# Kernel tuning notes

Measured on AMD Instinct MI355X. Metric: run time of the kernel, lower is better.

## Reference

```python
import jax, jax.numpy as jnp
import numpy as np

HID = 512       # hidden_dim (embed/LSTM input)
HDE = 512       # hidden_dim_de == attn_channels (required by conv_att channel count)
NCLS = 7000
LSEQ = 40
B = 128
FH, FW = 8, 32


def setup_inputs() -> dict:
    key = jax.random.key(0)
    ks = jax.random.split(key, 16)
    s = 0.05
    inp = {
        "hidden_en": jax.random.normal(ks[0], (1, B, HID), jnp.float32),
        "x_em": jax.random.normal(ks[1], (B, HDE, FH, FW), jnp.float32),
        "att_x_em": jax.random.normal(ks[2], (B, FH * FW, HDE), jnp.float32),
        "target": jax.random.randint(ks[3], (B, LSEQ), 0, NCLS),
        "feature_h": FH,
        "feature_w": FW,
        # parameters
        "embed_w": jax.random.normal(ks[4], (NCLS, HID), jnp.float32) * s,
        "W_ih": jax.random.normal(ks[5], (4 * HDE, HID), jnp.float32) * s,   # LSTMCell input weights (i,f,g,o)
        "W_hh": jax.random.normal(ks[6], (4 * HDE, HDE), jnp.float32) * s,
        "b_ih": jax.random.normal(ks[7], (4 * HDE,), jnp.float32) * s,
        "b_hh": jax.random.normal(ks[8], (4 * HDE,), jnp.float32) * s,
        "hem_w": jax.random.normal(ks[9], (HDE, HDE), jnp.float32) * s,     # 1x1 conv h_em as matrix
        "hem_b": jax.random.normal(ks[10], (HDE,), jnp.float32) * s,
        "attw_w": jax.random.normal(ks[11], (HDE,), jnp.float32) * s,       # 1x1 conv conv_att -> 1 channel
        "attw_b": jax.random.normal(ks[12], (), jnp.float32) * s,
        "lin_w": jax.random.normal(ks[13], (NCLS, HDE + HDE), jnp.float32) * s,
        "lin_b": jax.random.normal(ks[14], (NCLS,), jnp.float32) * s,
    }
    return inp


def _decode(hidden_en, x_em, att_x_em, target, embed_w, W_ih, W_hh, b_ih, b_hh,
            hem_w, hem_b, attw_w, attw_b, lin_w, lin_b):
    L = target.shape[1]
    # teacher-forced inputs: step 0 uses hidden_en[-1], step t>=1 uses embed(target[:, t-1])
    xt0 = hidden_en[-1]                                   # [B, HID]
    xts = jnp.concatenate([xt0[None], jnp.transpose(embed_w[target[:, : L - 1]], (1, 0, 2))], axis=0)  # [L,B,HID]
    xg_all = jnp.einsum('lbi,gi->lbg', xts, W_ih) + b_ih  # precompute input gates [L,B,4H]
    Bn = x_em.shape[0]
    h0 = jnp.zeros((Bn, HDE), x_em.dtype)
    c0 = jnp.zeros((Bn, HDE), x_em.dtype)

    def step(carry, xg):
        h, c = carry
        gates = xg + h @ W_hh.T + b_hh
        i, f, g, o = jnp.split(gates, 4, axis=-1)
        c = jax.nn.sigmoid(f) * c + jax.nn.sigmoid(i) * jnp.tanh(g)
        h = jax.nn.sigmoid(o) * jnp.tanh(c)
        # additive attention (dropout treated as identity for determinism)
        hem = h @ hem_w.T + hem_b                          # [B, C]
        feat = jnp.tanh(x_em + hem[:, :, None, None])      # [B, C, H, W]
        feat_att = jnp.einsum('bchw,c->bhw', feat, attw_w) + attw_b
        alpha = jax.nn.softmax(feat_att.reshape(Bn, -1), axis=-1)  # [B, HW]
        att = jnp.einsum('bn,bnd->bd', alpha, att_x_em)    # [B, C]
        scores = jax.nn.log_softmax(jnp.concatenate([h, att], -1) @ lin_w.T + lin_b)
        return (h, c), scores

    _, ys = jax.lax.scan(step, (h0, c0), xg_all)           # ys: [L, B, NCLS]
    return jnp.transpose(ys, (1, 0, 2))                    # [B, L, NCLS]


def reference(hidden_en, x_em, att_x_em, target, feature_h, feature_w,
              embed_w, W_ih, W_hh, b_ih, b_hh, hem_w, hem_b, attw_w, attw_b,
              lin_w, lin_b):
    return _decode(hidden_en, x_em, att_x_em, target, embed_w, W_ih, W_hh,
                   b_ih, b_hh, hem_w, hem_b, attw_w, attw_b, lin_w, lin_b)
```

## Files before the change

### kernel.cpp

```cpp
#include <hip/hip_runtime.h>

#define B_    128
#define HIDD  512
#define NCLS  7000
#define NPAD  7040
#define LSEQ  40
#define MROWS 5120
#define TT    10

typedef __attribute__((ext_vector_type(8))) short bf16x8;
typedef __attribute__((ext_vector_type(4))) float f32x4;

__device__ __forceinline__ unsigned short f2bf(float x) {
  union { float f; unsigned u; } v; v.f = x;
  unsigned r = v.u + 0x7fffu + ((v.u >> 16) & 1u);
  return (unsigned short)(r >> 16);
}
__device__ __forceinline__ float bf2f(unsigned short h) {
  union { unsigned u; float f; } v; v.u = ((unsigned)h) << 16;
  return v.f;
}
__device__ __forceinline__ float sigm(float x) { return 1.f / (1.f + __expf(-x)); }
__device__ __forceinline__ float tanh_f(float x) {
  float e = __expf(2.f * x);
  return 1.f - 2.f / (e + 1.f);
}
__device__ __forceinline__ float rcp_f(float x) { return __builtin_amdgcn_rcpf(x); }

__global__ __launch_bounds__(256) void k_cvt(const float* __restrict__ src,
                                             unsigned short* __restrict__ dst, int n4) {
  int i = blockIdx.x * 256 + threadIdx.x;
  if (i >= n4) return;
  float4 v = ((const float4*)src)[i];
  ushort4 o; o.x = f2bf(v.x); o.y = f2bf(v.y); o.z = f2bf(v.z); o.w = f2bf(v.w);
  ((ushort4*)dst)[i] = o;
}

__global__ __launch_bounds__(256) void k_expcvt(const float* __restrict__ src,
                                                unsigned short* __restrict__ dst, int n4) {
  int i = blockIdx.x * 256 + threadIdx.x;
  if (i >= n4) return;
  float4 v = ((const float4*)src)[i];
  ushort4 o;
  o.x = f2bf(__expf(2.f * v.x)); o.y = f2bf(__expf(2.f * v.y));
  o.z = f2bf(__expf(2.f * v.z)); o.w = f2bf(__expf(2.f * v.w));
  ((ushort4*)dst)[i] = o;
}

__global__ __launch_bounds__(256) void k_linpad(const float* __restrict__ lw,
                                                unsigned short* __restrict__ dst) {
  int i = blockIdx.x * 256 + threadIdx.x;
  int e = i * 4;
  int row = e >> 10;
  ushort4 o;
  if (row < NCLS) {
    float4 v = *(const float4*)(lw + (size_t)row * 1024 + (e & 1023));
    o.x = f2bf(v.x); o.y = f2bf(v.y); o.z = f2bf(v.z); o.w = f2bf(v.w);
  } else { o.x = 0; o.y = 0; o.z = 0; o.w = 0; }
  ((ushort4*)dst)[i] = o;
}

__global__ __launch_bounds__(256) void k_xts(const float* __restrict__ hidden_en,
                                             const float* __restrict__ embed_w,
                                             const int* __restrict__ target,
                                             unsigned short* __restrict__ xts) {
  int i = blockIdx.x * 256 + threadIdx.x;
  int e = i * 4;
  int r = e >> 9, col = e & 511;
  int l = r >> 7, b = r & 127;
  const float* src;
  if (l == 0) src = hidden_en + b * 512 + col;
  else        src = embed_w + (size_t)target[b * LSEQ + (l - 1)] * 512 + col;
  float4 v = *(const float4*)src;
  ushort4 o; o.x = f2bf(v.x); o.y = f2bf(v.y); o.z = f2bf(v.z); o.w = f2bf(v.w);
  ((ushort4*)xts)[i] = o;
}

template <int MODE>
__global__ __launch_bounds__(256) void k_gemm(const unsigned short* __restrict__ A, int lda,
                                              const unsigned short* __restrict__ Bw, int ldb,
                                              const float* __restrict__ bias,
                                              void* __restrict__ outp, int ldc, int K) {
  __shared__ __align__(16) unsigned short As[128 * 32];
  __shared__ __align__(16) unsigned short Bs[128 * 32];
  const int tid = threadIdx.x;
  const int lane = tid & 63, wid = tid >> 6;
  const int wm = wid >> 1, wn = wid & 1;
  const int quad = lane >> 4, l16 = lane & 15;
  const int m0 = blockIdx.x * 128, n0 = blockIdx.y * 128;
  f32x4 acc[4][4];
#pragma unroll
  for (int i = 0; i < 4; i++)
#pragma unroll
    for (int j = 0; j < 4; j++) acc[i][j] = (f32x4){0.f, 0.f, 0.f, 0.f};

  const int r0 = tid >> 2, kq0 = (tid & 3) * 8;
  for (int k0 = 0; k0 < K; k0 += 32) {
#pragma unroll
    for (int s = 0; s < 2; s++) {
      int row = r0 + s * 64;
      *(bf16x8*)(As + row * 32 + kq0) = *(const bf16x8*)(A + (size_t)(m0 + row) * lda + k0 + kq0);
      *(bf16x8*)(Bs + row * 32 + kq0) = *(const bf16x8*)(Bw + (size_t)(n0 + row) * ldb + k0 + kq0);
    }
    __syncthreads();
    bf16x8 af[4], bfr[4];
#pragma unroll
    for (int i = 0; i < 4; i++)
      af[i] = *(const bf16x8*)(As + (wm * 64 + i * 16 + l16) * 32 + quad * 8);
#pragma unroll
    for (int j = 0; j < 4; j++)
      bfr[j] = *(const bf16x8*)(Bs + (wn * 64 + j * 16 + l16) * 32 + quad * 8);
#pragma unroll
    for (int i = 0; i < 4; i++)
#pragma unroll
      for (int j = 0; j < 4; j++)
        acc[i][j] = __builtin_amdgcn_mfma_f32_16x16x32_bf16(af[i], bfr[j], acc[i][j], 0, 0, 0);
    __syncthreads();
  }
#pragma unroll
  for (int i = 0; i < 4; i++) {
    int mbase = m0 + wm * 64 + i * 16 + quad * 4;
#pragma unroll
    for (int j = 0; j < 4; j++) {
      int n = n0 + wn * 64 + j * 16 + l16;
#pragma unroll
      for (int r = 0; r < 4; r++) {
        float v = acc[i][j][r];
        int m = mbase + r;
        if (MODE == 0) {
          ((unsigned short*)outp)[(size_t)m * ldc + n] = f2bf(v + bias[n]);
        } else if (MODE == 3) {
          ((float*)outp)[(size_t)m * ldc + n] = __expf(2.f * (v + bias[n]));
        } else {
          if (n < NCLS) {
            int t = m >> 7, b = m & 127;
            ((float*)outp)[((size_t)(b * LSEQ + t)) * NCLS + n] = v + bias[n];
          }
        }
      }
    }
  }
}

__global__ __launch_bounds__(256) void k_gates(const float* __restrict__ h_prev,
                                               float* __restrict__ h_new,
                                               float* __restrict__ c_buf,
                                               const unsigned short* __restrict__ xg,
                                               const float* __restrict__ W_hh,
                                               const float* __restrict__ b_hh,
                                               unsigned short* __restrict__ hatt, int t) {
  __shared__ float h_s[16][68];
  __shared__ float W_s[64][68];
  const int tid = threadIdx.x;
  const int mt = blockIdx.x >> 5, jt = blockIdx.x & 31;
  const int m0 = mt * 16, j0 = jt * 16;
  const int mi = tid >> 4, ji = tid & 15;
  float a0 = 0.f, a1 = 0.f, a2 = 0.f, a3 = 0.f;
  if (t > 0) {
    for (int k0 = 0; k0 < 512; k0 += 64) {
      {
        int row = tid >> 4, c4 = (tid & 15) * 4;
        *(float4*)&h_s[row][c4] = *(const float4*)&h_prev[(m0 + row) * 512 + k0 + c4];
      }
#pragma unroll
      for (int w = 0; w < 4; w++) {
        int lin = w * 256 + tid;
        int row = lin >> 4, c4 = (lin & 15) * 4;
        int g = row >> 4, jj = row & 15;
        *(float4*)&W_s[row][c4] = *(const float4*)&W_hh[(size_t)((g << 9) + j0 + jj) * 512 + k0 + c4];
      }
      __syncthreads();
#pragma unroll 4
      for (int kk = 0; kk < 64; kk += 4) {
        float4 hv = *(const float4*)&h_s[mi][kk];
        float4 w0 = *(const float4*)&W_s[ji][kk];
        float4 w1 = *(const float4*)&W_s[16 + ji][kk];
        float4 w2 = *(const float4*)&W_s[32 + ji][kk];
        float4 w3 = *(const float4*)&W_s[48 + ji][kk];
        a0 += hv.x * w0.x + hv.y * w0.y + hv.z * w0.z + hv.w * w0.w;
        a1 += hv.x * w1.x + hv.y * w1.y + hv.z * w1.z + hv.w * w1.w;
        a2 += hv.x * w2.x + hv.y * w2.y + hv.z * w2.z + hv.w * w2.w;
        a3 += hv.x * w3.x + hv.y * w3.y + hv.z * w3.z + hv.w * w3.w;
      }
      __syncthreads();
    }
  }
  const int m = m0 + mi, j = j0 + ji;
  const size_t r = (size_t)t * 128 + m;
  a0 += bf2f(xg[r * 2048 + j])          + b_hh[j];
  a1 += bf2f(xg[r * 2048 + 512 + j])    + b_hh[512 + j];
  a2 += bf2f(xg[r * 2048 + 1024 + j])   + b_hh[1024 + j];
  a3 += bf2f(xg[r * 2048 + 1536 + j])   + b_hh[1536 + j];
  float ig = sigm(a0), fg = sigm(a1), gg = tanh_f(a2), og = sigm(a3);
  float c_old = (t > 0) ? c_buf[m * 512 + j] : 0.f;
  float c = fg * c_old + ig * gg;
  float h = og * tanh_f(c);
  c_buf[m * 512 + j] = c;
  h_new[m * 512 + j] = h;
  hatt[r * 1024 + j] = f2bf(h);
}

__global__ __launch_bounds__(256) void k_feat(const float* __restrict__ Eh,
                                              const unsigned short* __restrict__ Ex,
                                              const float* __restrict__ attw_w,
                                              float* __restrict__ s_all) {
  __shared__ float EhL[TT][512];
  __shared__ float wL[512];
  const int tid = threadIdx.x;
  const int tg = blockIdx.x >> 7, b = blockIdx.x & 127;
  const int t0 = tg * TT;
  for (int i = tid * 4; i < TT * 512; i += 1024) {
    int t = i >> 9, c = i & 511;
    *(float4*)&EhL[t][c] = *(const float4*)&Eh[((size_t)(t0 + t) * 128 + b) * 512 + c];
  }
  if (tid < 128) *(float4*)&wL[tid * 4] = *(const float4*)&attw_w[tid * 4];
  __syncthreads();
  const int p = tid;
  const unsigned short* xp = Ex + (size_t)b * 512 * 256 + p;
  float acc[TT];
#pragma unroll
  for (int t = 0; t < TT; t++) acc[t] = 0.f;
  for (int c0 = 0; c0 < 512; c0 += 4) {
    float ex0 = bf2f(xp[(size_t)(c0 + 0) * 256]);
    float ex1 = bf2f(xp[(size_t)(c0 + 1) * 256]);
    float ex2 = bf2f(xp[(size_t)(c0 + 2) * 256]);
    float ex3 = bf2f(xp[(size_t)(c0 + 3) * 256]);
    float4 wv = *(const float4*)&wL[c0];
#pragma unroll
    for (int t = 0; t < TT; t++) {
      float4 eh = *(const float4*)&EhL[t][c0];
      acc[t] = __builtin_fmaf(wv.x, rcp_f(__builtin_fmaf(ex0, eh.x, 1.f)), acc[t]);
      acc[t] = __builtin_fmaf(wv.y, rcp_f(__builtin_fmaf(ex1, eh.y, 1.f)), acc[t]);
      acc[t] = __builtin_fmaf(wv.z, rcp_f(__builtin_fmaf(ex2, eh.z, 1.f)), acc[t]);
      acc[t] = __builtin_fmaf(wv.w, rcp_f(__builtin_fmaf(ex3, eh.w, 1.f)), acc[t]);
    }
  }
#pragma unroll
  for (int t = 0; t < TT; t++)
    s_all[((size_t)(t0 + t) * 128 + b) * 256 + p] = -2.f * acc[t];
}

__global__ __launch_bounds__(256) void k_att(const float* __restrict__ s_all,
                                             const float* __restrict__ atx,
                                             unsigned short* __restrict__ hatt) {
  __shared__ float sL[40][257];
  __shared__ float zinv[40];
  const int tid = threadIdx.x;
  const int b = blockIdx.x >> 1, dh = blockIdx.x & 1;
  for (int i = tid; i < 40 * 256; i += 256) {
    int t = i >> 8, p = i & 255;
    sL[t][p] = s_all[((size_t)t * 128 + b) * 256 + p];
  }
  __syncthreads();
  if (tid < 40) {
    int t = tid;
    float mx = -1e30f;
    for (int p = 0; p < 256; p++) mx = fmaxf(mx, sL[t][p]);
    float z = 0.f;
    for (int p = 0; p < 256; p++) { float e = __expf(sL[t][p] - mx); sL[t][p] = e; z += e; }
    zinv[t] = 1.f / z;
  }
  __syncthreads();
  float acc[40];
#pragma unroll
  for (int t = 0; t < 40; t++) acc[t] = 0.f;
  const int d = dh * 256 + tid;
  const float* ap = atx + (size_t)b * 256 * 512 + d;
  for (int p = 0; p < 256; p++) {
    float av = ap[(size_t)p * 512];
#pragma unroll
    for (int t = 0; t < 40; t++) acc[t] += sL[t][p] * av;
  }
#pragma unroll
  for (int t = 0; t < 40; t++) {
    float v = acc[t] * zinv[t];
    hatt[((size_t)t * 128 + b) * 1024 + 512 + d] = f2bf(v);
  }
}

__global__ __launch_bounds__(256) void k_lsm(float* __restrict__ out) {
  __shared__ float buf[7000];
  __shared__ float red[256];
  const int tid = threadIdx.x;
  float* pr = out + (size_t)blockIdx.x * NCLS;
  for (int i = tid * 4; i < NCLS; i += 1024)
    *(float4*)&buf[i] = *(const float4*)&pr[i];
  __syncthreads();
  float mx = -1e30f;
  for (int i = tid; i < NCLS; i += 256) mx = fmaxf(mx, buf[i]);
  red[tid] = mx; __syncthreads();
  for (int s = 128; s > 0; s >>= 1) { if (tid < s) red[tid] = fmaxf(red[tid], red[tid + s]); __syncthreads(); }
  mx = red[0]; __syncthreads();
  float sum = 0.f;
  for (int i = tid; i < NCLS; i += 256) sum += __expf(buf[i] - mx);
  red[tid] = sum; __syncthreads();
  for (int s = 128; s > 0; s >>= 1) { if (tid < s) red[tid] += red[tid + s]; __syncthreads(); }
  float lse = mx + __logf(red[0]);
  for (int i = tid * 4; i < NCLS; i += 1024) {
    float4 v = *(const float4*)&buf[i];
    v.x -= lse; v.y -= lse; v.z -= lse; v.w -= lse;
    *(float4*)&pr[i] = v;
  }
}

extern "C" void kernel_launch(void* const* d_in, const int* in_sizes, int n_in,
                              void* d_out, int out_size, void* d_ws, size_t ws_size,
                              hipStream_t stream) {
  const float* hidden_en = (const float*)d_in[0];
  const float* x_em      = (const float*)d_in[1];
  const float* att_x     = (const float*)d_in[2];
  const int*   target    = (const int*)d_in[3];
  const float* embed_w   = (const float*)d_in[6];
  const float* W_ih      = (const float*)d_in[7];
  const float* W_hh      = (const float*)d_in[8];
  const float* b_ih      = (const float*)d_in[9];
  const float* b_hh      = (const float*)d_in[10];
  const float* hem_w     = (const float*)d_in[11];
  const float* hem_b     = (const float*)d_in[12];
  const float* attw_w    = (const float*)d_in[13];
  const float* lin_w     = (const float*)d_in[15];
  const float* lin_b     = (const float*)d_in[16];
  float* out = (float*)d_out;
  (void)in_sizes; (void)n_in; (void)out_size; (void)ws_size;

  char* w = (char*)d_ws;
  size_t off = 0;
  auto alloc = [&](size_t bytes) { char* p = w + off; off = (off + bytes + 255) & ~(size_t)255; return p; };
  unsigned short* xts  = (unsigned short*)alloc((size_t)MROWS * 512 * 2);
  unsigned short* wih  = (unsigned short*)alloc((size_t)2048 * 512 * 2);
  unsigned short* xg   = (unsigned short*)alloc((size_t)MROWS * 2048 * 2);
  unsigned short* hemw = (unsigned short*)alloc((size_t)512 * 512 * 2);
  unsigned short* linw = (unsigned short*)alloc((size_t)NPAD * 1024 * 2);
  unsigned short* xem  = (unsigned short*)alloc((size_t)128 * 512 * 256 * 2);
  unsigned short* hatt = (unsigned short*)alloc((size_t)MROWS * 1024 * 2);
  float* h0      = (float*)alloc((size_t)128 * 512 * 4);
  float* h1      = (float*)alloc((size_t)128 * 512 * 4);
  float* cb      = (float*)alloc((size_t)128 * 512 * 4);
  float* eh_all  = (float*)alloc((size_t)MROWS * 512 * 4);
  float* s_all   = (float*)alloc((size_t)MROWS * 256 * 4);

  k_cvt<<<1024, 256, 0, stream>>>(W_ih, wih, 2048 * 512 / 4);
  k_cvt<<<256, 256, 0, stream>>>(hem_w, hemw, 512 * 512 / 4);
  k_expcvt<<<16384, 256, 0, stream>>>(x_em, xem, 128 * 512 * 256 / 4);
  k_linpad<<<NPAD * 1024 / 4 / 256, 256, 0, stream>>>(lin_w, linw);
  k_xts<<<MROWS * 512 / 4 / 256, 256, 0, stream>>>(hidden_en, embed_w, target, xts);
  k_gemm<0><<<dim3(40, 16), 256, 0, stream>>>(xts, 512, wih, 512, b_ih, xg, 2048, 512);

  for (int t = 0; t < LSEQ; t++) {
    const float* hp = (t & 1) ? h0 : h1;
    float* hn = (t & 1) ? h1 : h0;
    k_gates<<<256, 256, 0, stream>>>(hp, hn, cb, xg, W_hh, b_hh, hatt, t);
  }

  k_gemm<3><<<dim3(40, 4), 256, 0, stream>>>(hatt, 1024, hemw, 512, hem_b, eh_all, 512, 512);
  k_feat<<<512, 256, 0, stream>>>(eh_all, xem, attw_w, s_all);
  k_att<<<256, 256, 0, stream>>>(s_all, att_x, hatt);

  k_gemm<2><<<dim3(40, 55), 256, 0, stream>>>(hatt, 1024, linw, 1024, lin_b, out, NCLS, 1024);
  k_lsm<<<MROWS, 256, 0, stream>>>(out);
}
```

Before: 1.394 ms.

## Replace per-step LSTM gate launches with a persistent cooperative scan kernel

Replaces the 40 separate k_gates launches with a single cooperative kernel that loops over time steps and uses grid.sync between them. Each block keeps its slice of W_hh (64 rows x 512 floats) resident in LDS and holds the cell state in a register, which removes the per-step reload of recurrent weights, the launch overhead and the c_buf round-trip. It falls back to the old per-step launches if the cooperative launch fails. The cost is about 132KB of LDS per block, which needs all 256 blocks to be co-resident, plus the grid-wide barrier latency at every step.

```diff
diff --git a/kernel.cpp b/kernel.cpp
--- a/kernel.cpp
+++ b/kernel.cpp
@@ -1,4 +1,7 @@
 #include <hip/hip_runtime.h>
+#include <hip/hip_cooperative_groups.h>
+
+namespace cg = cooperative_groups;
 
 #define B_    128
 #define HIDD  512
@@ -198,6 +201,69 @@
   c_buf[m * 512 + j] = c;
   h_new[m * 512 + j] = h;
   hatt[r * 1024 + j] = f2bf(h);
+}
+
+__global__ __launch_bounds__(256) void k_scan(float* __restrict__ h0,
+                                              float* __restrict__ h1,
+                                              const unsigned short* __restrict__ xg,
+                                              const float* __restrict__ W_hh,
+                                              const float* __restrict__ b_hh,
+                                              unsigned short* __restrict__ hatt) {
+  cg::grid_group grid = cg::this_grid();
+  __shared__ float W_s[64][516];
+  __shared__ float h_s[16][68];
+  const int tid = threadIdx.x;
+  const int mt = blockIdx.x >> 5, jt = blockIdx.x & 31;
+  const int m0 = mt * 16, j0 = jt * 16;
+  const int mi = tid >> 4, ji = tid & 15;
+  const int m = m0 + mi, j = j0 + ji;
+
+  for (int i = tid; i < 64 * 128; i += 256) {
+    int row = i >> 7, c4 = (i & 127) * 4;
+    int g = row >> 4, jj = row & 15;
+    *(float4*)&W_s[row][c4] = *(const float4*)&W_hh[(size_t)((g << 9) + j0 + jj) * 512 + c4];
+  }
+  __syncthreads();
+
+  float cc = 0.f;
+  for (int t = 0; t < LSEQ; t++) {
+    const float* h_prev = (t & 1) ? h0 : h1;
+    float* h_new = (t & 1) ? h1 : h0;
+    float a0 = 0.f, a1 = 0.f, a2 = 0.f, a3 = 0.f;
+    if (t > 0) {
+      for (int k0 = 0; k0 < 512; k0 += 64) {
+        {
+          int row = tid >> 4, c4 = (tid & 15) * 4;
+          *(float4*)&h_s[row][c4] = *(const float4*)&h_prev[(m0 + row) * 512 + k0 + c4];
+        }
+        __syncthreads();
+#pragma unroll 4
+        for (int kk = 0; kk < 64; kk += 4) {
+          float4 hv = *(const float4*)&h_s[mi][kk];
+          float4 w0 = *(const float4*)&W_s[ji][k0 + kk];
+          float4 w1 = *(const float4*)&W_s[16 + ji][k0 + kk];
+          float4 w2 = *(const float4*)&W_s[32 + ji][k0 + kk];
+          float4 w3 = *(const float4*)&W_s[48 + ji][k0 + kk];
+          a0 += hv.x * w0.x + hv.y * w0.y + hv.z * w0.z + hv.w * w0.w;
+          a1 += hv.x * w1.x + hv.y * w1.y + hv.z * w1.z + hv.w * w1.w;
+          a2 += hv.x * w2.x + hv.y * w2.y + hv.z * w2.z + hv.w * w2.w;
+          a3 += hv.x * w3.x + hv.y * w3.y + hv.z * w3.z + hv.w * w3.w;
+        }
+        __syncthreads();
+      }
+    }
+    const size_t r = (size_t)t * 128 + m;
+    a0 += bf2f(xg[r * 2048 + j])          + b_hh[j];
+    a1 += bf2f(xg[r * 2048 + 512 + j])    + b_hh[512 + j];
+    a2 += bf2f(xg[r * 2048 + 1024 + j])   + b_hh[1024 + j];
+    a3 += bf2f(xg[r * 2048 + 1536 + j])   + b_hh[1536 + j];
+    float ig = sigm(a0), fg = sigm(a1), gg = tanh_f(a2), og = sigm(a3);
+    cc = fg * cc + ig * gg;
+    float h = og * tanh_f(cc);
+    h_new[m * 512 + j] = h;
+    hatt[r * 1024 + j] = f2bf(h);
+    if (t < LSEQ - 1) grid.sync();
+  }
 }
 
 __global__ __launch_bounds__(256) void k_feat(const float* __restrict__ Eh,
@@ -346,10 +412,16 @@
   k_xts<<<MROWS * 512 / 4 / 256, 256, 0, stream>>>(hidden_en, embed_w, target, xts);
   k_gemm<0><<<dim3(40, 16), 256, 0, stream>>>(xts, 512, wih, 512, b_ih, xg, 2048, 512);
 
-  for (int t = 0; t < LSEQ; t++) {
-    const float* hp = (t & 1) ? h0 : h1;
-    float* hn = (t & 1) ? h1 : h0;
-    k_gates<<<256, 256, 0, stream>>>(hp, hn, cb, xg, W_hh, b_hh, hatt, t);
+  {
+    void* args[] = { (void*)&h0, (void*)&h1, (void*)&xg, (void*)&W_hh, (void*)&b_hh, (void*)&hatt };
+    hipError_t ce = hipLaunchCooperativeKernel(k_scan, dim3(256), dim3(256), args, 0u, stream);
+    if (ce != hipSuccess) {
+      for (int t = 0; t < LSEQ; t++) {
+        const float* hp = (t & 1) ? h0 : h1;
+        float* hn = (t & 1) ? h1 : h0;
+        k_gates<<<256, 256, 0, stream>>>(hp, hn, cb, xg, W_hh, b_hh, hatt, t);
+      }
+    }
   }
 
   k_gemm<3><<<dim3(40, 4), 256, 0, stream>>>(hatt, 1024, hemw, 512, hem_b, eh_all, 512, 512);
```

New measurement: 2.477 ms. +77.6%, slower.

## Fuse LSTM recurrence into one persistent MFMA kernel with permuted gate weights

Applied to the files above, without the earlier changes.

Replaces the 40 per-step fp32 gate kernel launches with a single persistent kernel of 8 blocks, each owning 16 batch rows for all timesteps. The hidden state stays in swizzled LDS and the cell state stays in registers, and W_hh is fed to bf16 MFMA from a gate-interleaved permuted copy. W_ih is permuted the same way and b_ih+b_hh are pre-summed into the input-gate GEMM bias. This removes launch overhead and global round trips of h/c, but uses only 8 CUs, rereads W_hh from L2 every step, and drops the recurrent matmul to bf16.

```diff
diff --git a/kernel.cpp b/kernel.cpp
--- a/kernel.cpp
+++ b/kernel.cpp
@@ -34,6 +34,21 @@
   float4 v = ((const float4*)src)[i];
   ushort4 o; o.x = f2bf(v.x); o.y = f2bf(v.y); o.z = f2bf(v.z); o.w = f2bf(v.w);
   ((ushort4*)dst)[i] = o;
+}
+
+__global__ __launch_bounds__(256) void k_cvtp(const float* __restrict__ src,
+                                              unsigned short* __restrict__ dst,
+                                              const float* __restrict__ b1,
+                                              const float* __restrict__ b2,
+                                              float* __restrict__ bsum) {
+  int i = blockIdx.x * 256 + threadIdx.x;
+  int e = i * 4;
+  int n = e >> 9, col = e & 511;
+  int srow = (n & 3) * 512 + (n >> 7) * 32 + ((n >> 4) & 7) * 4 + ((n >> 2) & 3);
+  float4 v = *(const float4*)(src + (size_t)srow * 512 + col);
+  ushort4 o; o.x = f2bf(v.x); o.y = f2bf(v.y); o.z = f2bf(v.z); o.w = f2bf(v.w);
+  ((ushort4*)dst)[i] = o;
+  if (bsum != nullptr && col == 0) bsum[n] = b1[srow] + b2[srow];
 }
 
 __global__ __launch_bounds__(256) void k_expcvt(const float* __restrict__ src,
@@ -142,62 +157,57 @@
   }
 }
 
-__global__ __launch_bounds__(256) void k_gates(const float* __restrict__ h_prev,
-                                               float* __restrict__ h_new,
-                                               float* __restrict__ c_buf,
-                                               const unsigned short* __restrict__ xg,
-                                               const float* __restrict__ W_hh,
-                                               const float* __restrict__ b_hh,
-                                               unsigned short* __restrict__ hatt, int t) {
-  __shared__ float h_s[16][68];
-  __shared__ float W_s[64][68];
-  const int tid = threadIdx.x;
-  const int mt = blockIdx.x >> 5, jt = blockIdx.x & 31;
-  const int m0 = mt * 16, j0 = jt * 16;
-  const int mi = tid >> 4, ji = tid & 15;
-  float a0 = 0.f, a1 = 0.f, a2 = 0.f, a3 = 0.f;
-  if (t > 0) {
-    for (int k0 = 0; k0 < 512; k0 += 64) {
-      {
-        int row = tid >> 4, c4 = (tid & 15) * 4;
-        *(float4*)&h_s[row][c4] = *(const float4*)&h_prev[(m0 + row) * 512 + k0 + c4];
-      }
-#pragma unroll
-      for (int w = 0; w < 4; w++) {
-        int lin = w * 256 + tid;
-        int row = lin >> 4, c4 = (lin & 15) * 4;
-        int g = row >> 4, jj = row & 15;
-        *(float4*)&W_s[row][c4] = *(const float4*)&W_hh[(size_t)((g << 9) + j0 + jj) * 512 + k0 + c4];
+__global__ __launch_bounds__(1024) void k_scan2(const unsigned short* __restrict__ whhp,
+                                                const unsigned short* __restrict__ xg,
+                                                unsigned short* __restrict__ hatt) {
+  __shared__ __align__(16) unsigned short Hl[16 * 512];
+  const int tid = threadIdx.x;
+  const int lane = tid & 63, w = tid >> 6;
+  const int quad = lane >> 4, l16 = lane & 15;
+  const int m0 = blockIdx.x * 16;
+  const unsigned short* wbase = whhp + ((size_t)(w * 128 + l16) * 512) + quad * 8;
+
+  f32x4 acc[8];
+  float cst[8];
+#pragma unroll
+  for (int i = 0; i < 8; i++) cst[i] = 0.f;
+
+  for (int t = 0; t < LSEQ; t++) {
+#pragma unroll
+    for (int i = 0; i < 8; i++) acc[i] = (f32x4){0.f, 0.f, 0.f, 0.f};
+    if (t > 0) {
+#pragma unroll
+      for (int ks = 0; ks < 16; ks++) {
+        bf16x8 hf = *(const bf16x8*)((const char*)Hl +
+                     ((l16 * 1024 + ks * 64 + quad * 16) ^ ((l16 & 7) << 4)));
+#pragma unroll
+        for (int nt = 0; nt < 8; nt++) {
+          bf16x8 wf = *(const bf16x8*)(wbase + nt * 8192 + ks * 32);
+          acc[nt] = __builtin_amdgcn_mfma_f32_16x16x32_bf16(wf, hf, acc[nt], 0, 0, 0);
+        }
       }
       __syncthreads();
-#pragma unroll 4
-      for (int kk = 0; kk < 64; kk += 4) {
-        float4 hv = *(const float4*)&h_s[mi][kk];
-        float4 w0 = *(const float4*)&W_s[ji][kk];
-        float4 w1 = *(const float4*)&W_s[16 + ji][kk];
-        float4 w2 = *(const float4*)&W_s[32 + ji][kk];
-        float4 w3 = *(const float4*)&W_s[48 + ji][kk];
-        a0 += hv.x * w0.x + hv.y * w0.y + hv.z * w0.z + hv.w * w0.w;
-        a1 += hv.x * w1.x + hv.y * w1.y + hv.z * w1.z + hv.w * w1.w;
-        a2 += hv.x * w2.x + hv.y * w2.y + hv.z * w2.z + hv.w * w2.w;
-        a3 += hv.x * w3.x + hv.y * w3.y + hv.z * w3.z + hv.w * w3.w;
-      }
-      __syncthreads();
-    }
-  }
-  const int m = m0 + mi, j = j0 + ji;
-  const size_t r = (size_t)t * 128 + m;
-  a0 += bf2f(xg[r * 2048 + j])          + b_hh[j];
-  a1 += bf2f(xg[r * 2048 + 512 + j])    + b_hh[512 + j];
-  a2 += bf2f(xg[r * 2048 + 1024 + j])   + b_hh[1024 + j];
-  a3 += bf2f(xg[r * 2048 + 1536 + j])   + b_hh[1536 + j];
-  float ig = sigm(a0), fg = sigm(a1), gg = tanh_f(a2), og = sigm(a3);
-  float c_old = (t > 0) ? c_buf[m * 512 + j] : 0.f;
-  float c = fg * c_old + ig * gg;
-  float h = og * tanh_f(c);
-  c_buf[m * 512 + j] = c;
-  h_new[m * 512 + j] = h;
-  hatt[r * 1024 + j] = f2bf(h);
+    }
+    const size_t xrow = (size_t)(t * 128 + m0 + l16);
+    const unsigned short* xp = xg + xrow * 2048 + w * 128 + quad * 4;
+    unsigned short* hp = hatt + xrow * 1024;
+#pragma unroll
+    for (int nt = 0; nt < 8; nt++) {
+      ushort4 xv = *(const ushort4*)(xp + nt * 16);
+      float ip = acc[nt].x + bf2f(xv.x);
+      float fp = acc[nt].y + bf2f(xv.y);
+      float gp = acc[nt].z + bf2f(xv.z);
+      float op = acc[nt].w + bf2f(xv.w);
+      float c = sigm(fp) * cst[nt] + sigm(ip) * tanh_f(gp);
+      cst[nt] = c;
+      float h = sigm(op) * tanh_f(c);
+      unsigned short hb = f2bf(h);
+      int j = w * 32 + nt * 4 + quad;
+      hp[j] = hb;
+      *(unsigned short*)((char*)Hl + ((l16 * 1024 + j * 2) ^ ((l16 & 7) << 4))) = hb;
+    }
+    __syncthreads();
+  }
 }
 
 __global__ __launch_bounds__(256) void k_feat(const float* __restrict__ Eh,
@@ -327,30 +337,26 @@
   size_t off = 0;
   auto alloc = [&](size_t bytes) { char* p = w + off; off = (off + bytes + 255) & ~(size_t)255; return p; };
   unsigned short* xts  = (unsigned short*)alloc((size_t)MROWS * 512 * 2);
-  unsigned short* wih  = (unsigned short*)alloc((size_t)2048 * 512 * 2);
+  unsigned short* wihp = (unsigned short*)alloc((size_t)2048 * 512 * 2);
+  unsigned short* whhp = (unsigned short*)alloc((size_t)2048 * 512 * 2);
   unsigned short* xg   = (unsigned short*)alloc((size_t)MROWS * 2048 * 2);
   unsigned short* hemw = (unsigned short*)alloc((size_t)512 * 512 * 2);
   unsigned short* linw = (unsigned short*)alloc((size_t)NPAD * 1024 * 2);
   unsigned short* xem  = (unsigned short*)alloc((size_t)128 * 512 * 256 * 2);
   unsigned short* hatt = (unsigned short*)alloc((size_t)MROWS * 1024 * 2);
-  float* h0      = (float*)alloc((size_t)128 * 512 * 4);
-  float* h1      = (float*)alloc((size_t)128 * 512 * 4);
-  float* cb      = (float*)alloc((size_t)128 * 512 * 4);
+  float* bsum    = (float*)alloc((size_t)2048 * 4);
   float* eh_all  = (float*)alloc((size_t)MROWS * 512 * 4);
   float* s_all   = (float*)alloc((size_t)MROWS * 256 * 4);
 
-  k_cvt<<<1024, 256, 0, stream>>>(W_ih, wih, 2048 * 512 / 4);
+  k_cvtp<<<1024, 256, 0, stream>>>(W_ih, wihp, b_ih, b_hh, bsum);
+  k_cvtp<<<1024, 256, 0, stream>>>(W_hh, whhp, nullptr, nullptr, nullptr);
   k_cvt<<<256, 256, 0, stream>>>(hem_w, hemw, 512 * 512 / 4);
   k_expcvt<<<16384, 256, 0, stream>>>(x_em, xem, 128 * 512 * 256 / 4);
   k_linpad<<<NPAD * 1024 / 4 / 256, 256, 0, stream>>>(lin_w, linw);
   k_xts<<<MROWS * 512 / 4 / 256, 256, 0, stream>>>(hidden_en, embed_w, target, xts);
-  k_gemm<0><<<dim3(40, 16), 256, 0, stream>>>(xts, 512, wih, 512, b_ih, xg, 2048, 512);
-
-  for (int t = 0; t < LSEQ; t++) {
-    const float* hp = (t & 1) ? h0 : h1;
-    float* hn = (t & 1) ? h1 : h0;
-    k_gates<<<256, 256, 0, stream>>>(hp, hn, cb, xg, W_hh, b_hh, hatt, t);
-  }
+  k_gemm<0><<<dim3(40, 16), 256, 0, stream>>>(xts, 512, wihp, 512, bsum, xg, 2048, 512);
+
+  k_scan2<<<8, 1024, 0, stream>>>(whhp, xg, hatt);
 
   k_gemm<3><<<dim3(40, 4), 256, 0, stream>>>(hatt, 1024, hemw, 512, hem_b, eh_all, 512, 512);
   k_feat<<<512, 256, 0, stream>>>(eh_all, xem, attw_w, s_all);
```

Result: slower. 3.857 ms (+176.6%).
